# Optimization experiments

Measured on AMD Instinct MI355X. Metric: run time of the kernel, lower is better.

## Reference

```python
import jax, jax.numpy as jnp
import numpy as np

N = 100000       # nodes
E = 1600000      # edges (avg degree 16)
D_IN = 6         # in_node_dim
HID = 128        # hidden_dim (heads=1)
OUT = 2          # output_dim
NEG_SLOPE = 0.2  # PyG GATConv leaky_relu slope


def setup_inputs() -> dict:
    key = jax.random.key(0)
    ks = jax.random.split(key, 16)
    inp = {
        "x": jax.random.normal(ks[0], (N, D_IN), dtype=jnp.float32),
        "edge_index": jax.random.randint(ks[1], (2, E), 0, N, dtype=jnp.int64),
        "edge_weight": jax.random.uniform(ks[2], (E, 1), dtype=jnp.float32),
        # GATConv params (heads=1, out=HID)
        "w_gat": jax.random.normal(ks[3], (D_IN, HID), dtype=jnp.float32) * 0.1,
        "att_src": jax.random.normal(ks[4], (HID,), dtype=jnp.float32) * 0.1,
        "att_dst": jax.random.normal(ks[5], (HID,), dtype=jnp.float32) * 0.1,
        "w_edge": jax.random.normal(ks[6], (1, HID), dtype=jnp.float32) * 0.1,
        "att_edge": jax.random.normal(ks[7], (HID,), dtype=jnp.float32) * 0.1,
        "b_gat": jax.random.normal(ks[8], (HID,), dtype=jnp.float32) * 0.01,
        # GCNConv params
        "w_gcn": jax.random.normal(ks[9], (HID, HID), dtype=jnp.float32) * 0.05,
        "b_gcn": jax.random.normal(ks[10], (HID,), dtype=jnp.float32) * 0.01,
        # output Linear
        "w_out": jax.random.normal(ks[11], (HID, OUT), dtype=jnp.float32) * 0.05,
        "b_out": jax.random.normal(ks[12], (OUT,), dtype=jnp.float32) * 0.01,
    }
    return inp


def _segment_softmax(logits, seg, num_segments):
    # numerically stable softmax over edges grouped by destination node
    m = jax.ops.segment_max(logits, seg, num_segments=num_segments)
    m = jnp.where(jnp.isfinite(m), m, 0.0)  # empty segments
    e = jnp.exp(logits - m[seg])
    denom = jax.ops.segment_sum(e, seg, num_segments=num_segments)
    return e / jnp.clip(denom, 1e-16)[seg]


def reference(x, edge_weight, w_gat, att_src, att_dst, w_edge, att_edge,
              b_gat, w_gcn, b_gcn, w_out, b_out, edge_index):
    x = x.astype(jnp.float32)
    edge_weight = edge_weight.astype(jnp.float32)
    src, dst = edge_index[0], edge_index[1]

    # ---- GATConv (heads=1, edge_dim=1, no self loops) ----
    h = x @ w_gat                              # [N, HID]
    a_src = h @ att_src                        # [N]
    a_dst = h @ att_dst                        # [N]
    e_feat = edge_weight @ w_edge              # [E, HID]
    a_edge = e_feat @ att_edge                 # [E]
    logits = jax.nn.leaky_relu(a_src[src] + a_dst[dst] + a_edge, NEG_SLOPE)
    alpha = _segment_softmax(logits, dst, N)   # [E], attention weights
    h_gat = jax.ops.segment_sum(alpha[:, None] * h[src], dst, num_segments=N)
    h_gat = h_gat + b_gat                      # [N, HID]
    h1 = jax.nn.relu(h_gat)

    # ---- GCNConv with edge_weight = alpha (no self loops, symmetric norm) ----
    deg = jax.ops.segment_sum(alpha, dst, num_segments=N)  # [N]
    dinv = jnp.where(deg > 0, deg ** -0.5, 0.0)
    norm = dinv[src] * alpha * dinv[dst]       # [E]
    hx = h1 @ w_gcn                            # [N, HID]
    h2 = jax.ops.segment_sum(norm[:, None] * hx[src], dst, num_segments=N)
    h2 = jax.nn.relu(h2 + b_gcn)

    # ---- output head ----
    out = h2 @ w_out + b_out                   # [N, OUT]
    return out, edge_index, alpha
```

## Files before the change

### kernel.cpp

```cpp
#include <hip/hip_runtime.h>
#include <hip/hip_bf16.h>
#include <math.h>

#define N_NODES 100000
#define N_EDGES 1600000
#define HID 128
#define D_IN 6
#define NEG_SLOPE 0.2f

#define NB_BKT 128
#define NBKT 782
#define NBLK_P 256
#define EPB ((N_EDGES + NBLK_P - 1) / NBLK_P)
#define NHIST (NBKT * NBLK_P)
#define S2_CAP 3072

__global__ __launch_bounds__(128) void k_prep(
    const float* __restrict__ w_gat, const float* __restrict__ att_src,
    const float* __restrict__ att_dst, const float* __restrict__ w_edge,
    const float* __restrict__ att_edge, float* __restrict__ w_as,
    float* __restrict__ w_ad, float* __restrict__ dotwe)
{
    int tid = threadIdx.x;
    __shared__ float red[4];
    float as = att_src[tid], ad = att_dst[tid];

    float v = w_edge[tid] * att_edge[tid];
    for (int o = 32; o; o >>= 1) v += __shfl_down(v, o);
    if ((tid & 63) == 0) red[tid >> 6] = v;
    __syncthreads();
    if (tid == 0) dotwe[0] = red[0] + red[1];

#pragma unroll
    for (int i = 0; i < D_IN; ++i) {
        float wv = w_gat[i * HID + tid];
        float v1 = wv * as, v2 = wv * ad;
        for (int o = 32; o; o >>= 1) {
            v1 += __shfl_down(v1, o);
            v2 += __shfl_down(v2, o);
        }
        __syncthreads();
        if ((tid & 63) == 0) { red[(tid >> 6) * 2] = v1; red[(tid >> 6) * 2 + 1] = v2; }
        __syncthreads();
        if (tid == 0) { w_as[i] = red[0] + red[2]; w_ad[i] = red[1] + red[3]; }
    }
}

__global__ __launch_bounds__(256) void k_asrc(
    const float* __restrict__ x, const float* __restrict__ w_as,
    const float* __restrict__ w_ad, float* __restrict__ a_src,
    float* __restrict__ a_dst)
{
    int n = blockIdx.x * 256 + threadIdx.x;
    if (n >= N_NODES) return;
    float s0 = 0.f, s1 = 0.f;
#pragma unroll
    for (int i = 0; i < D_IN; ++i) {
        float xv = x[n * D_IN + i];
        s0 += xv * w_as[i];
        s1 += xv * w_ad[i];
    }
    a_src[n] = s0;
    a_dst[n] = s1;
}

__global__ __launch_bounds__(1024) void k_hist(
    const int* __restrict__ dst, int* __restrict__ histG)
{
    __shared__ int h[NBKT];
    for (int b = threadIdx.x; b < NBKT; b += 1024) h[b] = 0;
    __syncthreads();
    int e0 = blockIdx.x * EPB, e1 = min(e0 + EPB, N_EDGES);
    for (int e = e0 + threadIdx.x; e < e1; e += 1024)
        atomicAdd(&h[dst[e] >> 7], 1);
    __syncthreads();
    for (int b = threadIdx.x; b < NBKT; b += 1024)
        histG[b * NBLK_P + blockIdx.x] = h[b];
}

__global__ __launch_bounds__(512) void k_scan1(
    const int* __restrict__ in, int* __restrict__ incl, int* __restrict__ bsums,
    int n)
{
    __shared__ int s[512];
    int tid = threadIdx.x;
    int i = blockIdx.x * 512 + tid;
    int v = (i < n) ? in[i] : 0;
    s[tid] = v;
    __syncthreads();
    for (int o = 1; o < 512; o <<= 1) {
        int t = (tid >= o) ? s[tid - o] : 0;
        __syncthreads();
        s[tid] += t;
        __syncthreads();
    }
    if (i < n) incl[i] = s[tid];
    if (tid == 511) bsums[blockIdx.x] = s[511];
}

__global__ __launch_bounds__(512) void k_scan2(
    const int* __restrict__ bsums, int* __restrict__ boffs, int nb)
{
    __shared__ int s[512];
    int tid = threadIdx.x;
    int v = (tid < nb) ? bsums[tid] : 0;
    s[tid] = v;
    __syncthreads();
    for (int o = 1; o < 512; o <<= 1) {
        int t = (tid >= o) ? s[tid - o] : 0;
        __syncthreads();
        s[tid] += t;
        __syncthreads();
    }
    if (tid < nb) boffs[tid] = s[tid] - v;
}

__global__ __launch_bounds__(512) void k_scan3(
    const int* __restrict__ in, const int* __restrict__ incl,
    const int* __restrict__ boffs, int* __restrict__ off, int n)
{
    int i = blockIdx.x * 512 + threadIdx.x;
    if (i < n) {
        int b = boffs[blockIdx.x];
        off[i] = b + incl[i] - in[i];
        if (i == n - 1) off[n] = b + incl[i];
    }
}

__global__ __launch_bounds__(1024) void k_part(
    const int* __restrict__ src, const int* __restrict__ dst,
    const float* __restrict__ ew, const float* __restrict__ a_src,
    const float* __restrict__ a_dst, const float* __restrict__ dotwe,
    const int* __restrict__ offP, float* __restrict__ p_arr,
    uint2* __restrict__ rec)
{
    __shared__ int curs[NBKT];
    for (int b = threadIdx.x; b < NBKT; b += 1024)
        curs[b] = offP[b * NBLK_P + blockIdx.x];
    __syncthreads();
    float dw = dotwe[0];
    int e0 = blockIdx.x * EPB, e1 = min(e0 + EPB, N_EDGES);
    for (int e = e0 + threadIdx.x; e < e1; e += 1024) {
        int d = dst[e], s = src[e];
        float lg = a_src[s] + a_dst[d] + dw * ew[e];
        lg = (lg >= 0.f) ? lg : NEG_SLOPE * lg;
        float p = __expf(lg);
        p_arr[e] = p;
        int pos = atomicAdd(&curs[d >> 7], 1);
        rec[pos] = make_uint2(((unsigned)(d & 127) << 17) | (unsigned)s,
                              __float_as_uint(p));
    }
}

__global__ __launch_bounds__(256) void k_s2(
    const int* __restrict__ offP, const uint2* __restrict__ rec,
    const float* __restrict__ x, uint2* __restrict__ sa_srt,
    float* __restrict__ xagg8, float* __restrict__ denomG,
    int* __restrict__ off)
{
    __shared__ uint2 srt[S2_CAP];
    __shared__ int cntL[NB_BKT], fillL[NB_BKT], baseL[NB_BKT + 1];
    __shared__ int sc[NB_BKT];
    __shared__ float rden[NB_BKT];
    int b = blockIdx.x, tid = threadIdx.x;
    int g0 = offP[b * NBLK_P];
    int g1 = offP[(b + 1) * NBLK_P];
    int len = min(g1 - g0, S2_CAP);

    if (tid < NB_BKT) { cntL[tid] = 0; fillL[tid] = 0; }
    __syncthreads();

    for (int i = tid; i < len; i += 256)
        atomicAdd(&cntL[rec[g0 + i].x >> 17], 1);
    __syncthreads();

    {
        int v = (tid < NB_BKT) ? cntL[tid] : 0;
        if (tid < NB_BKT) sc[tid] = v;
        __syncthreads();
        for (int o = 1; o < NB_BKT; o <<= 1) {
            int t = (tid >= o && tid < NB_BKT) ? sc[tid - o] : 0;
            __syncthreads();
            if (tid < NB_BKT) sc[tid] += t;
            __syncthreads();
        }
        if (tid < NB_BKT) baseL[tid + 1] = sc[tid];
        if (tid == 0) baseL[0] = 0;
    }
    __syncthreads();

    for (int i = tid; i < len; i += 256) {
        uint2 r = rec[g0 + i];
        int dl = r.x >> 17;
        int p = baseL[dl] + atomicAdd(&fillL[dl], 1);
        if (p < S2_CAP) srt[p] = r;
    }
    __syncthreads();

    if (tid < NB_BKT) {
        int s0 = baseL[tid], s1 = baseL[tid + 1];
        float dsum = 0.f;
        for (int j = s0; j < s1; ++j) dsum += __uint_as_float(srt[j].y);
        int n = b * NB_BKT + tid;
        if (n < N_NODES) denomG[n] = dsum;
        rden[tid] = 1.0f / fmaxf(dsum, 1e-16f);
    }
    __syncthreads();

    for (int i = tid; i < len; i += 256) {
        uint2 r = srt[i];
        int dl = r.x >> 17;
        float a = __uint_as_float(r.y) * rden[dl];
        srt[i].y = __float_as_uint(a);
        sa_srt[g0 + i] = make_uint2(r.x & 0x1FFFFu, __float_as_uint(a));
    }
    __syncthreads();

    if (tid < NB_BKT) {
        int n = b * NB_BKT + tid;
        if (n < N_NODES) {
            int s0 = baseL[tid], s1 = baseL[tid + 1];
            float ax0 = 0, ax1 = 0, ax2 = 0, ax3 = 0, ax4 = 0, ax5 = 0;
            for (int j = s0; j < s1; ++j) {
                uint2 r = srt[j];
                float a = __uint_as_float(r.y);
                const float2* xp = (const float2*)(x + (size_t)(r.x & 0x1FFFFu) * D_IN);
                float2 q0 = xp[0], q1 = xp[1], q2 = xp[2];
                ax0 += a * q0.x; ax1 += a * q0.y; ax2 += a * q1.x;
                ax3 += a * q1.y; ax4 += a * q2.x; ax5 += a * q2.y;
            }
            float dv = (s1 > s0) ? 1.0f : 0.0f;
            float* xo = xagg8 + (size_t)n * 8;
            float4 lo = {dv, ax0, ax1, ax2};
            float4 hi = {ax3, ax4, ax5, 0.f};
            *(float4*)xo = lo;
            *(float4*)(xo + 4) = hi;
            off[n] = g0 + s0;
        }
    }
    if (b == NBKT - 1 && tid == 0) off[N_NODES] = g1;
}

__global__ __launch_bounds__(256) void k_alpha(
    const float* __restrict__ p_arr, const int* __restrict__ dst,
    const float* __restrict__ denomG, float* __restrict__ alpha_out)
{
    int e = blockIdx.x * 256 + threadIdx.x;
    if (e >= N_EDGES) return;
    alpha_out[e] = p_arr[e] / fmaxf(denomG[dst[e]], 1e-16f);
}

#define GCAP 256
__global__ __launch_bounds__(256) void k_gcn_gather(
    const uint2* __restrict__ sa_srt, const int* __restrict__ off,
    const float* __restrict__ xagg8, const float* __restrict__ w_gat,
    const float* __restrict__ b_gat, float* __restrict__ agg)
{
    __shared__ float lds[GCAP * 12];
    int tid = threadIdx.x;
    int n0 = blockIdx.x * 4;
    int wid = tid >> 6, l = tid & 63;
    int n = n0 + wid;
    int beg0 = off[n0];
    int total = off[n0 + 4] - beg0;
    int nb = off[n] - beg0, ne = off[n + 1] - beg0;

    int kA = l, kB = l + 64;
    float wA0 = w_gat[0 * HID + kA], wA1 = w_gat[1 * HID + kA], wA2 = w_gat[2 * HID + kA];
    float wA3 = w_gat[3 * HID + kA], wA4 = w_gat[4 * HID + kA], wA5 = w_gat[5 * HID + kA];
    float wB0 = w_gat[0 * HID + kB], wB1 = w_gat[1 * HID + kB], wB2 = w_gat[2 * HID + kB];
    float wB3 = w_gat[3 * HID + kB], wB4 = w_gat[4 * HID + kB], wB5 = w_gat[5 * HID + kB];
    float bA = b_gat[kA], bB = b_gat[kB];
    float accA = 0.f, accB = 0.f;

    for (int base = 0; base < total; base += GCAP) {
        int cnt = min(GCAP, total - base);
        __syncthreads();
        if (tid < cnt) {
            int j = beg0 + base + tid;
            uint2 sa = sa_srt[j];
            float a = __uint_as_float(sa.y);
            const float4* xp = (const float4*)(xagg8 + (size_t)sa.x * 8);
            float4 lo = xp[0], hi = xp[1];
            float4 w0 = {lo.x * a, lo.y, lo.z, lo.w};
            float4 w1 = {hi.x, hi.y, hi.z, 0.f};
            *(float4*)(lds + tid * 12) = w0;
            *(float4*)(lds + tid * 12 + 4) = w1;
        }
        __syncthreads();
        int lo_t = nb - base; if (lo_t < 0) lo_t = 0;
        int hi_t = ne - base; if (hi_t > cnt) hi_t = cnt;
        for (int t = lo_t; t < hi_t; ++t) {
            float4 e0 = *(const float4*)(lds + t * 12);
            float4 e1 = *(const float4*)(lds + t * 12 + 4);
            float hA = bA, hB = bB;
            hA = fmaf(e0.y, wA0, hA); hB = fmaf(e0.y, wB0, hB);
            hA = fmaf(e0.z, wA1, hA); hB = fmaf(e0.z, wB1, hB);
            hA = fmaf(e0.w, wA2, hA); hB = fmaf(e0.w, wB2, hB);
            hA = fmaf(e1.x, wA3, hA); hB = fmaf(e1.x, wB3, hB);
            hA = fmaf(e1.y, wA4, hA); hB = fmaf(e1.y, wB4, hB);
            hA = fmaf(e1.z, wA5, hA); hB = fmaf(e1.z, wB5, hB);
            hA = fmaxf(hA, 0.f); hB = fmaxf(hB, 0.f);
            accA = fmaf(e0.x, hA, accA); accB = fmaf(e0.x, hB, accB);
        }
    }
    float dn = xagg8[(size_t)n * 8];
    agg[(size_t)n * HID + kA] = dn * accA;
    agg[(size_t)n * HID + kB] = dn * accB;
}

#define DM 128
#define DK 32
__global__ __launch_bounds__(256, 4) void k_dense2(
    const float* __restrict__ agg, const float* __restrict__ w_gcn,
    const float* __restrict__ b_gcn, const float* __restrict__ w_out,
    const float* __restrict__ b_out, float* __restrict__ out)
{
    __shared__ float As[DK][DM + 4];
    __shared__ float Bs[DK][HID];
    int tid = threadIdx.x;
    int m0 = blockIdx.x * DM;
    int tx = tid & 15;
    int ty = tid >> 4;

    float acc[8][8];
#pragma unroll
    for (int r = 0; r < 8; ++r)
#pragma unroll
        for (int j = 0; j < 8; ++j) acc[r][j] = 0.f;

    for (int k0 = 0; k0 < HID; k0 += DK) {
#pragma unroll
        for (int q = 0; q < 4; ++q) {
            int idx4 = tid + q * 256;
            int m = idx4 >> 3;
            int k4 = (idx4 & 7) * 4;
            int gm = m0 + m;
            float4 v = (gm < N_NODES)
                ? *(const float4*)(agg + (size_t)gm * HID + k0 + k4)
                : make_float4(0.f, 0.f, 0.f, 0.f);
            As[k4 + 0][m] = v.x;
            As[k4 + 1][m] = v.y;
            As[k4 + 2][m] = v.z;
            As[k4 + 3][m] = v.w;
        }
#pragma unroll
        for (int q = 0; q < 4; ++q) {
            int idx4 = tid + q * 256;
            int k = idx4 >> 5;
            int n4 = (idx4 & 31) * 4;
            *(float4*)&Bs[k][n4] = *(const float4*)(w_gcn + (size_t)(k0 + k) * HID + n4);
        }
        __syncthreads();
#pragma unroll 4
        for (int k = 0; k < DK; ++k) {
            float4 w0 = *(const float4*)&Bs[k][tx * 8];
            float4 w1 = *(const float4*)&Bs[k][tx * 8 + 4];
            float4 h0 = *(const float4*)&As[k][ty * 8];
            float4 h1 = *(const float4*)&As[k][ty * 8 + 4];
            float hv[8] = {h0.x, h0.y, h0.z, h0.w, h1.x, h1.y, h1.z, h1.w};
            float wv[8] = {w0.x, w0.y, w0.z, w0.w, w1.x, w1.y, w1.z, w1.w};
#pragma unroll
            for (int r = 0; r < 8; ++r)
#pragma unroll
                for (int j = 0; j < 8; ++j)
                    acc[r][j] = fmaf(hv[r], wv[j], acc[r][j]);
        }
        __syncthreads();
    }

    float bb[8], wo0[8], wo1[8];
#pragma unroll
    for (int j = 0; j < 8; ++j) {
        int c = tx * 8 + j;
        bb[j] = b_gcn[c];
        wo0[j] = w_out[c * 2 + 0];
        wo1[j] = w_out[c * 2 + 1];
    }
#pragma unroll
    for (int r = 0; r < 8; ++r) {
        float p0 = 0.f, p1 = 0.f;
#pragma unroll
        for (int j = 0; j < 8; ++j) {
            float h2 = fmaxf(acc[r][j] + bb[j], 0.f);
            p0 = fmaf(h2, wo0[j], p0);
            p1 = fmaf(h2, wo1[j], p1);
        }
        p0 += __shfl_xor(p0, 1);  p1 += __shfl_xor(p1, 1);
        p0 += __shfl_xor(p0, 2);  p1 += __shfl_xor(p1, 2);
        p0 += __shfl_xor(p0, 4);  p1 += __shfl_xor(p1, 4);
        p0 += __shfl_xor(p0, 8);  p1 += __shfl_xor(p1, 8);
        if (tx == 0) {
            int gm = m0 + ty * 8 + r;
            if (gm < N_NODES) {
                out[(size_t)gm * 2 + 0] = p0 + b_out[0];
                out[(size_t)gm * 2 + 1] = p1 + b_out[1];
            }
        }
    }
}

__global__ __launch_bounds__(256) void k_copy_ei(
    const int* __restrict__ ei, float* __restrict__ out_ei)
{
    int i = blockIdx.x * 256 + threadIdx.x;
    if (i < (2 * N_EDGES) / 4) {
        int4 v = ((const int4*)ei)[i];
        float4 f = {(float)v.x, (float)v.y, (float)v.z, (float)v.w};
        ((float4*)out_ei)[i] = f;
    }
}

extern "C" void kernel_launch(void* const* d_in, const int* in_sizes, int n_in,
                              void* d_out, int out_size, void* d_ws, size_t ws_size,
                              hipStream_t stream)
{
    const float* x        = (const float*)d_in[0];
    const int*   ei       = (const int*)d_in[1];
    const float* ew       = (const float*)d_in[2];
    const float* w_gat    = (const float*)d_in[3];
    const float* att_src  = (const float*)d_in[4];
    const float* att_dst  = (const float*)d_in[5];
    const float* w_edge   = (const float*)d_in[6];
    const float* att_edge = (const float*)d_in[7];
    const float* b_gat    = (const float*)d_in[8];
    const float* w_gcn    = (const float*)d_in[9];
    const float* b_gcn    = (const float*)d_in[10];
    const float* w_out    = (const float*)d_in[11];
    const float* b_out    = (const float*)d_in[12];

    const int* src = ei;
    const int* dst = ei + N_EDGES;

    float* out_head  = (float*)d_out;
    float* out_ei    = out_head + 2 * N_NODES;
    float* out_alpha = out_ei + 2 * N_EDGES;

    char* ws = (char*)d_ws;
    size_t o = 0;
    auto alloc = [&](size_t bytes) -> char* {
        char* p = ws + o;
        o = (o + bytes + 255) & ~(size_t)255;
        return p;
    };
    float* agg    = (float*)alloc((size_t)N_NODES * HID * 4);
    uint2* rec    = (uint2*)alloc((size_t)N_EDGES * 8);
    uint2* sa_srt = (uint2*)alloc((size_t)N_EDGES * 8);
    float* p_arr  = (float*)alloc((size_t)N_EDGES * 4);
    float* xagg8  = (float*)alloc((size_t)N_NODES * 8 * 4);
    int*   histG  = (int*)alloc((size_t)NHIST * 4);
    int*   incl   = (int*)alloc((size_t)NHIST * 4);
    int*   offP   = (int*)alloc((size_t)(NHIST + 1) * 4);
    float* a_src  = (float*)alloc(N_NODES * 4);
    float* a_dst  = (float*)alloc(N_NODES * 4);
    float* denomG = (float*)alloc(N_NODES * 4);
    int*   off    = (int*)alloc((N_NODES + 1) * 4);
    int*   bsums  = (int*)alloc(512 * 4);
    int*   boffs  = (int*)alloc(512 * 4);
    float* w_as   = (float*)alloc(D_IN * 4);
    float* w_ad   = (float*)alloc(D_IN * 4);
    float* dotwe  = (float*)alloc(4);
    (void)ws_size; (void)out_size; (void)n_in; (void)in_sizes;

    const int NB_NODE = (N_NODES + 255) / 256;
    const int NB_EDGE = (N_EDGES + 255) / 256;
    const int NB_SCANP = (NHIST + 511) / 512;

    k_prep<<<1, 128, 0, stream>>>(w_gat, att_src, att_dst, w_edge, att_edge,
                                  w_as, w_ad, dotwe);
    k_asrc<<<NB_NODE, 256, 0, stream>>>(x, w_as, w_ad, a_src, a_dst);
    k_hist<<<NBLK_P, 1024, 0, stream>>>(dst, histG);
    k_scan1<<<NB_SCANP, 512, 0, stream>>>(histG, incl, bsums, NHIST);
    k_scan2<<<1, 512, 0, stream>>>(bsums, boffs, NB_SCANP);
    k_scan3<<<NB_SCANP, 512, 0, stream>>>(histG, incl, boffs, offP, NHIST);
    k_part<<<NBLK_P, 1024, 0, stream>>>(src, dst, ew, a_src, a_dst, dotwe,
                                        offP, p_arr, rec);
    k_s2<<<NBKT, 256, 0, stream>>>(offP, rec, x, sa_srt, xagg8, denomG, off);
    k_alpha<<<NB_EDGE, 256, 0, stream>>>(p_arr, dst, denomG, out_alpha);
    k_gcn_gather<<<N_NODES / 4, 256, 0, stream>>>(
        sa_srt, off, xagg8, w_gat, b_gat, agg);
    k_dense2<<<(N_NODES + DM - 1) / DM, 256, 0, stream>>>(
        agg, w_gcn, b_gcn, w_out, b_out, out_head);
    k_copy_ei<<<(2 * N_EDGES) / 4 / 256 + 1, 256, 0, stream>>>(ei, out_ei);
}
```

Baseline: 297.5 us.

## Give each wave private LDS staging in GCN gather and drop block barriers

Each wave stages and consumes the edges of its own destination node in a private LDS slice, so the block-wide __syncthreads and shared edge window across four nodes go away. The inner loop handles two edges per iteration with paired float2 FMAs, and blocks grow to 512 threads covering eight nodes. This targets barrier stalls and imbalance between waves with different degrees. It relies on intra-wave ordering of LDS write/read and uses more LDS per block.

```diff
diff --git a/kernel.cpp b/kernel.cpp
--- a/kernel.cpp
+++ b/kernel.cpp
@@ -14,6 +14,10 @@
 #define EPB ((N_EDGES + NBLK_P - 1) / NBLK_P)
 #define NHIST (NBKT * NBLK_P)
 #define S2_CAP 3072
+
+__device__ inline float2 fma2(float s, float2 w, float2 c) {
+    return make_float2(fmaf(s, w.x, c.x), fmaf(s, w.y, c.y));
+}
 
 __global__ __launch_bounds__(128) void k_prep(
     const float* __restrict__ w_gat, const float* __restrict__ att_src,
@@ -250,63 +254,73 @@
     alpha_out[e] = p_arr[e] / fmaxf(denomG[dst[e]], 1e-16f);
 }
 
-#define GCAP 256
-__global__ __launch_bounds__(256) void k_gcn_gather(
+#define WCAP 64
+__global__ __launch_bounds__(512) void k_gcn_gather(
     const uint2* __restrict__ sa_srt, const int* __restrict__ off,
     const float* __restrict__ xagg8, const float* __restrict__ w_gat,
     const float* __restrict__ b_gat, float* __restrict__ agg)
 {
-    __shared__ float lds[GCAP * 12];
+    __shared__ float lds[8][WCAP * 12];
     int tid = threadIdx.x;
-    int n0 = blockIdx.x * 4;
-    int wid = tid >> 6, l = tid & 63;
-    int n = n0 + wid;
-    int beg0 = off[n0];
-    int total = off[n0 + 4] - beg0;
-    int nb = off[n] - beg0, ne = off[n + 1] - beg0;
-
-    int kA = l, kB = l + 64;
-    float wA0 = w_gat[0 * HID + kA], wA1 = w_gat[1 * HID + kA], wA2 = w_gat[2 * HID + kA];
-    float wA3 = w_gat[3 * HID + kA], wA4 = w_gat[4 * HID + kA], wA5 = w_gat[5 * HID + kA];
-    float wB0 = w_gat[0 * HID + kB], wB1 = w_gat[1 * HID + kB], wB2 = w_gat[2 * HID + kB];
-    float wB3 = w_gat[3 * HID + kB], wB4 = w_gat[4 * HID + kB], wB5 = w_gat[5 * HID + kB];
-    float bA = b_gat[kA], bB = b_gat[kB];
-    float accA = 0.f, accB = 0.f;
-
-    for (int base = 0; base < total; base += GCAP) {
-        int cnt = min(GCAP, total - base);
-        __syncthreads();
-        if (tid < cnt) {
-            int j = beg0 + base + tid;
-            uint2 sa = sa_srt[j];
+    int w = tid >> 6, l = tid & 63;
+    int n = blockIdx.x * 8 + w;
+    int beg = off[n], end = off[n + 1];
+    float* reg = lds[w];
+
+    float2 wp[D_IN], bp;
+#pragma unroll
+    for (int i = 0; i < D_IN; ++i)
+        wp[i] = make_float2(w_gat[i * HID + l], w_gat[i * HID + l + 64]);
+    bp = make_float2(b_gat[l], b_gat[l + 64]);
+    float2 acc = make_float2(0.f, 0.f);
+
+    for (int base = beg; base < end; base += WCAP) {
+        int cnt = min(WCAP, end - base);
+        if (l < cnt) {
+            uint2 sa = sa_srt[base + l];
             float a = __uint_as_float(sa.y);
             const float4* xp = (const float4*)(xagg8 + (size_t)sa.x * 8);
             float4 lo = xp[0], hi = xp[1];
             float4 w0 = {lo.x * a, lo.y, lo.z, lo.w};
             float4 w1 = {hi.x, hi.y, hi.z, 0.f};
-            *(float4*)(lds + tid * 12) = w0;
-            *(float4*)(lds + tid * 12 + 4) = w1;
-        }
-        __syncthreads();
-        int lo_t = nb - base; if (lo_t < 0) lo_t = 0;
-        int hi_t = ne - base; if (hi_t > cnt) hi_t = cnt;
-        for (int t = lo_t; t < hi_t; ++t) {
-            float4 e0 = *(const float4*)(lds + t * 12);
-            float4 e1 = *(const float4*)(lds + t * 12 + 4);
-            float hA = bA, hB = bB;
-            hA = fmaf(e0.y, wA0, hA); hB = fmaf(e0.y, wB0, hB);
-            hA = fmaf(e0.z, wA1, hA); hB = fmaf(e0.z, wB1, hB);
-            hA = fmaf(e0.w, wA2, hA); hB = fmaf(e0.w, wB2, hB);
-            hA = fmaf(e1.x, wA3, hA); hB = fmaf(e1.x, wB3, hB);
-            hA = fmaf(e1.y, wA4, hA); hB = fmaf(e1.y, wB4, hB);
-            hA = fmaf(e1.z, wA5, hA); hB = fmaf(e1.z, wB5, hB);
-            hA = fmaxf(hA, 0.f); hB = fmaxf(hB, 0.f);
-            accA = fmaf(e0.x, hA, accA); accB = fmaf(e0.x, hB, accB);
+            *(float4*)(reg + l * 12) = w0;
+            *(float4*)(reg + l * 12 + 4) = w1;
+        }
+        int t = 0;
+        for (; t + 2 <= cnt; t += 2) {
+            float4 a0 = *(const float4*)(reg + t * 12);
+            float4 a1 = *(const float4*)(reg + t * 12 + 4);
+            float4 b0 = *(const float4*)(reg + (t + 1) * 12);
+            float4 b1 = *(const float4*)(reg + (t + 1) * 12 + 4);
+            float2 hA = bp, hB = bp;
+            hA = fma2(a0.y, wp[0], hA);  hB = fma2(b0.y, wp[0], hB);
+            hA = fma2(a0.z, wp[1], hA);  hB = fma2(b0.z, wp[1], hB);
+            hA = fma2(a0.w, wp[2], hA);  hB = fma2(b0.w, wp[2], hB);
+            hA = fma2(a1.x, wp[3], hA);  hB = fma2(b1.x, wp[3], hB);
+            hA = fma2(a1.y, wp[4], hA);  hB = fma2(b1.y, wp[4], hB);
+            hA = fma2(a1.z, wp[5], hA);  hB = fma2(b1.z, wp[5], hB);
+            hA.x = fmaxf(hA.x, 0.f); hA.y = fmaxf(hA.y, 0.f);
+            hB.x = fmaxf(hB.x, 0.f); hB.y = fmaxf(hB.y, 0.f);
+            acc = fma2(a0.x, hA, acc);
+            acc = fma2(b0.x, hB, acc);
+        }
+        if (t < cnt) {
+            float4 a0 = *(const float4*)(reg + t * 12);
+            float4 a1 = *(const float4*)(reg + t * 12 + 4);
+            float2 hA = bp;
+            hA = fma2(a0.y, wp[0], hA);
+            hA = fma2(a0.z, wp[1], hA);
+            hA = fma2(a0.w, wp[2], hA);
+            hA = fma2(a1.x, wp[3], hA);
+            hA = fma2(a1.y, wp[4], hA);
+            hA = fma2(a1.z, wp[5], hA);
+            hA.x = fmaxf(hA.x, 0.f); hA.y = fmaxf(hA.y, 0.f);
+            acc = fma2(a0.x, hA, acc);
         }
     }
     float dn = xagg8[(size_t)n * 8];
-    agg[(size_t)n * HID + kA] = dn * accA;
-    agg[(size_t)n * HID + kB] = dn * accB;
+    agg[(size_t)n * HID + l] = dn * acc.x;
+    agg[(size_t)n * HID + l + 64] = dn * acc.y;
 }
 
 #define DM 128
@@ -477,7 +491,7 @@
                                         offP, p_arr, rec);
     k_s2<<<NBKT, 256, 0, stream>>>(offP, rec, x, sa_srt, xagg8, denomG, off);
     k_alpha<<<NB_EDGE, 256, 0, stream>>>(p_arr, dst, denomG, out_alpha);
-    k_gcn_gather<<<N_NODES / 4, 256, 0, stream>>>(
+    k_gcn_gather<<<N_NODES / 8, 512, 0, stream>>>(
         sa_srt, off, xagg8, w_gat, b_gat, agg);
     k_dense2<<<(N_NODES + DM - 1) / DM, 256, 0, stream>>>(
         agg, w_gcn, b_gcn, w_out, b_out, out_head);
```

Result: no change. 295.1 us (-0.8%).
